# Performance work log

Hardware: AMD Instinct MI355X
Metric: run time of the kernel (lower is better)

Reference implementation:

```python
import math
import jax, jax.numpy as jnp
import numpy as np
from jax import lax

PATCHSIZE = [(8, 8), (4, 4), (2, 2), (1, 1)]  # (width, height)
BN_EPS = 1e-5


def setup_inputs() -> dict:
    key = jax.random.key(0)
    ks = jax.random.split(key, 6)
    b, c, h, w = 4, 256, 64, 64
    s = 1.0 / math.sqrt(c)
    return {
        "x": jax.random.normal(ks[0], (b, c, h, w), jnp.float32),
        "Wq": jax.random.normal(ks[1], (c, c), jnp.float32) * s,
        "bq": jnp.zeros((c,), jnp.float32),
        "Wk": jax.random.normal(ks[2], (c, c), jnp.float32) * s,
        "bk": jnp.zeros((c,), jnp.float32),
        "Wv": jax.random.normal(ks[3], (c, c), jnp.float32) * s,
        "bv": jnp.zeros((c,), jnp.float32),
        "Wo": jax.random.normal(ks[4], (c, c, 3, 3), jnp.float32) * (1.0 / math.sqrt(c * 9)),
        "bo": jnp.zeros((c,), jnp.float32),
        "gamma": jnp.ones((c,), jnp.float32),
        "beta": jnp.zeros((c,), jnp.float32),
        "running_mean": jnp.zeros((c,), jnp.float32),
        "running_var": jnp.ones((c,), jnp.float32),
    }


def _patch_attention(q, k, v, ph, pw):
    # q/k/v: [b, dk, h, w] -> tokens [b, n_patches, dk*ph*pw]
    b, dk, h, w = q.shape
    oh, ow = h // ph, w // pw

    def to_tok(t):
        t = t.reshape(b, dk, oh, ph, ow, pw)
        return t.transpose(0, 2, 4, 1, 3, 5).reshape(b, oh * ow, dk * ph * pw)

    qt, kt, vt = to_tok(q), to_tok(k), to_tok(v)
    scale = 1.0 / math.sqrt(dk * ph * pw)
    scores = jnp.einsum("bnd,bmd->bnm", qt, kt) * scale
    y = jnp.einsum("bnm,bmd->bnd", jax.nn.softmax(scores, axis=-1), vt)
    y = y.reshape(b, oh, ow, dk, ph, pw).transpose(0, 3, 1, 4, 2, 5)
    return y.reshape(b, dk, h, w)


def reference(x, Wq, bq, Wk, bk, Wv, bv, Wo, bo, gamma, beta, running_mean, running_var):
    b, c, h, w = x.shape
    nh = len(PATCHSIZE)
    dk = c // nh
    # 1x1 conv QKV projections
    q = jnp.einsum("bchw,oc->bohw", x, Wq) + bq[:, None, None]
    k = jnp.einsum("bchw,oc->bohw", x, Wk) + bk[:, None, None]
    v = jnp.einsum("bchw,oc->bohw", x, Wv) + bv[:, None, None]
    outs = []
    for i, (pw_, ph_) in enumerate(PATCHSIZE):
        sl = slice(i * dk, (i + 1) * dk)
        outs.append(_patch_attention(q[:, sl], k[:, sl], v[:, sl], ph_, pw_))
    out = jnp.concatenate(outs, axis=1)
    # 3x3 conv, SAME padding
    out = lax.conv_general_dilated(
        out, Wo, window_strides=(1, 1), padding="SAME",
        dimension_numbers=("NCHW", "OIHW", "NCHW"),
    ) + bo[:, None, None]
    # BatchNorm2d (inference-mode with running stats)
    inv = lax.rsqrt(running_var + BN_EPS)
    out = (out - running_mean[:, None, None]) * (gamma * inv)[:, None, None] + beta[:, None, None]
    # LeakyReLU(0.2)
    return jnp.where(out >= 0, out, 0.2 * out)
```

## Files before the change

kernel.cpp:

```cpp
#include <hip/hip_runtime.h>
#include <hip/hip_bf16.h>
#include <math.h>

#define NPOS 4096
#define CPB  1048576
#define QOFF  ((size_t)0)
#define KOFF  ((size_t)4194304)
#define VOFF  ((size_t)8388608)
#define AOFF  ((size_t)12582912)
#define S0OFF ((size_t)16777216)
#define WTOFF ((size_t)21250048)
#define QTOFF   S0OFF
#define KTOFF   (S0OFF + (size_t)2097152)
#define SP0OFF  (S0OFF + (size_t)4194304)
#define VTOFF   QOFF
#define ML3OFF  (QOFF + (size_t)2097152)
#define ML2OFF  (QOFF + (size_t)2228224)
#define OP3OFF  KOFF
#define SP1OFF  VOFF
#define OP2OFF  (VOFF + (size_t)2097152)

#define LOG2E 1.44269504088896340736f

typedef __attribute__((ext_vector_type(8))) short bf16x8;
typedef __attribute__((ext_vector_type(4))) float f32x4;

static __device__ __forceinline__ unsigned short f2bf(float f) {
  __hip_bfloat16 h = __float2bfloat16(f);
  unsigned short u;
  __builtin_memcpy(&u, &h, sizeof(u));
  return u;
}

static __device__ __forceinline__ float bf2f(unsigned short u) {
  unsigned v = ((unsigned)u) << 16;
  float f;
  __builtin_memcpy(&f, &v, sizeof(f));
  return f;
}

template<int PH, int PW>
__device__ __forceinline__ void scat_qk(unsigned short* __restrict__ dst,
                                        const unsigned short* __restrict__ Ac,
                                        int gh, int tid) {
  constexpr int PP = PH * PW, OW = 64 / PW, D = 64 * PP;
  int po = gh / PH, y = gh % PH;
  constexpr int NCH = 64 * OW;
#pragma unroll
  for (int j = 0; j < NCH / 256; ++j) {
    int id = j * 256 + tid;
    int c = id / OW, qo = id % OW;
    int tt = po * OW + qo;
    unsigned short buf[PW];
#pragma unroll
    for (int x = 0; x < PW; ++x) buf[x] = Ac[c * 66 + qo * PW + x];
    unsigned short* dp = &dst[(size_t)tt * D + c * PP + y * PW];
    if constexpr (PW == 8)      { uint4 v;  __builtin_memcpy(&v, buf, 16); *(uint4*)dp = v; }
    else if constexpr (PW == 4) { uint2 v;  __builtin_memcpy(&v, buf, 8);  *(uint2*)dp = v; }
    else                        { unsigned v; __builtin_memcpy(&v, buf, 4); *(unsigned*)dp = v; }
  }
}

template<int PH, int PW>
__device__ __forceinline__ void scat_v(unsigned short* __restrict__ dst,
                                       const unsigned short* __restrict__ Ac,
                                       int gh, int tid) {
  constexpr int PP = PH * PW, OW = 64 / PW, NT = 4096 / PP;
  int po = gh / PH, y = gh % PH;
  constexpr int NCH = 64 * PW;
  constexpr int CPT = (NCH + 255) / 256;
#pragma unroll
  for (int j = 0; j < CPT; ++j) {
    int id = j * 256 + tid;
    if (NCH < 256 && id >= NCH) break;
    int c = id / PW, x = id % PW;
    int d = c * PP + y * PW + x;
    unsigned short* dp = &dst[(size_t)d * NT + po * OW];
#pragma unroll
    for (int s = 0; s < OW; s += 8) {
      unsigned short buf[8];
#pragma unroll
      for (int e = 0; e < 8; ++e) buf[e] = Ac[c * 66 + (s + e) * PW + x];
      uint4 v; __builtin_memcpy(&v, buf, 16);
      *(uint4*)&dp[s] = v;
    }
  }
}

__global__ __launch_bounds__(256) void qkv_fused(
    const float* __restrict__ x,
    const float* __restrict__ Wq, const float* __restrict__ Wk, const float* __restrict__ Wv,
    const float* __restrict__ bq, const float* __restrict__ bk, const float* __restrict__ bv,
    const float* __restrict__ Wo, unsigned short* __restrict__ W2,
    unsigned short* __restrict__ qt, unsigned short* __restrict__ kt_,
    unsigned short* __restrict__ vt) {
  if (blockIdx.z == 12) {
    int o = blockIdx.y * 64 + blockIdx.x;
    size_t base = (size_t)o * 2304;
#pragma unroll
    for (int r = 0; r < 9; ++r) {
      int rr = r * 256 + threadIdx.x;
      int c = rr / 9, k = rr % 9;
      W2[(size_t)k * 65536 + (size_t)o * 256 + c] = f2bf(Wo[base + rr]);
    }
    return;
  }
  int b = blockIdx.z / 3, t = blockIdx.z % 3;
  const float* W    = (t == 0) ? Wq : (t == 1) ? Wk : Wv;
  const float* bias = (t == 0) ? bq : (t == 1) ? bk : bv;
  int h = blockIdx.y, gh = blockIdx.x;
  int o0 = h * 64, p0 = gh * 64;
  __shared__ unsigned short smem[2 * 64 * 72];
  unsigned short* Wt = smem;
  unsigned short* Xs = smem + 64 * 72;
  int tid = threadIdx.x;
  int wv = tid >> 6, l = tid & 63;
  int lg = l >> 4, ll = l & 15;
  f32x4 acc[4];
#pragma unroll
  for (int mi = 0; mi < 4; ++mi) acc[mi] = (f32x4){0.f, 0.f, 0.f, 0.f};

  int wol = tid >> 2, wcp = (tid & 3) * 16;
  int xcc = tid >> 6, xpz = tid & 63;

  for (int c0 = 0; c0 < 256; c0 += 64) {
    __syncthreads();
#pragma unroll
    for (int u = 0; u < 4; ++u) {
      float4 w4 = *(const float4*)&W[(size_t)(o0 + wol) * 256 + c0 + wcp + u * 4];
      ushort4 pk;
      pk.x = f2bf(w4.x); pk.y = f2bf(w4.y); pk.z = f2bf(w4.z); pk.w = f2bf(w4.w);
      *(ushort4*)&Wt[wol * 72 + wcp + u * 4] = pk;
    }
#pragma unroll
    for (int r = 0; r < 16; ++r) {
      int c = xcc * 16 + r;
      Xs[xpz * 72 + c] = f2bf(x[(size_t)b * CPB + (size_t)(c0 + c) * NPOS + p0 + xpz]);
    }
    __syncthreads();
#pragma unroll
    for (int ks = 0; ks < 2; ++ks) {
      bf16x8 xb = *(const bf16x8*)&Xs[(wv * 16 + ll) * 72 + ks * 32 + lg * 8];
#pragma unroll
      for (int mi = 0; mi < 4; ++mi) {
        bf16x8 wa = *(const bf16x8*)&Wt[(mi * 16 + ll) * 72 + ks * 32 + lg * 8];
        acc[mi] = __builtin_amdgcn_mfma_f32_16x16x32_bf16(wa, xb, acc[mi], 0, 0, 0);
      }
    }
  }
  __syncthreads();
  float qs = 1.0f;
  if (t == 0) qs = (h == 2) ? 0.0625f * LOG2E : (h == 3) ? 0.125f * LOG2E : 1.0f;
  unsigned short* Ac = smem;
#pragma unroll
  for (int mi = 0; mi < 4; ++mi)
#pragma unroll
    for (int r = 0; r < 4; ++r) {
      int ol = mi * 16 + lg * 4 + r;
      Ac[ol * 66 + wv * 16 + ll] = f2bf((acc[mi][r] + bias[o0 + ol]) * qs);
    }
  __syncthreads();
  if (t < 2) {
    unsigned short* dst = (t == 0 ? qt : kt_) + ((size_t)b * 4 + h) * 262144;
    switch (h) {
      case 0: scat_qk<8, 8>(dst, Ac, gh, tid); break;
      case 1: scat_qk<4, 4>(dst, Ac, gh, tid); break;
      case 2: scat_qk<2, 2>(dst, Ac, gh, tid); break;
      default: {
        int p = tid >> 2, c0 = (tid & 3) * 16;
        unsigned short buf[16];
#pragma unroll
        for (int e = 0; e < 16; ++e) buf[e] = Ac[(c0 + e) * 66 + p];
        uint4 v0, v1;
        __builtin_memcpy(&v0, buf, 16);
        __builtin_memcpy(&v1, buf + 8, 16);
        uint4* d4 = (uint4*)&dst[(size_t)(gh * 64 + p) * 64 + c0];
        d4[0] = v0; d4[1] = v1;
      } break;
    }
  } else {
    unsigned short* dst = vt + ((size_t)b * 4 + h) * 262144;
    switch (h) {
      case 0: scat_v<8, 8>(dst, Ac, gh, tid); break;
      case 1: scat_v<4, 4>(dst, Ac, gh, tid); break;
      case 2: scat_v<2, 2>(dst, Ac, gh, tid); break;
      default: {
        if (tid < 64) {
#pragma unroll
          for (int seg = 0; seg < 8; ++seg) {
            unsigned short buf[8];
#pragma unroll
            for (int e = 0; e < 8; ++e) buf[e] = Ac[tid * 66 + seg * 8 + e];
            uint4 v; __builtin_memcpy(&v, buf, 16);
            *(uint4*)&dst[(size_t)tid * 4096 + gh * 64 + seg * 8] = v;
          }
        }
      } break;
    }
  }
}

template<int NTOK, int DDIM, int NSPLIT, int KVB, int PH, int PW, int HEAD>
__device__ __forceinline__ void flash_body(
    unsigned char* smem, int b, int q0, int split,
    const unsigned short* __restrict__ qt, const unsigned short* __restrict__ kt_,
    const unsigned short* __restrict__ vt, unsigned short* __restrict__ opart,
    float* __restrict__ ml, unsigned short* __restrict__ attbf) {
  constexpr int KSTR = DDIM + 8;
  constexpr int VSTR = KVB + 8;
  constexpr int NT   = KVB / 16;
  constexpr int KCH  = DDIM / 32;
  constexpr int PKS  = KVB / 32;
  constexpr int OCG  = DDIM / 16;
  constexpr int PP = PH * PW, OW = 64 / PW;
  const unsigned short* Q = qt + ((size_t)b * 4 + HEAD) * 262144;
  const unsigned short* K = kt_ + ((size_t)b * 4 + HEAD) * 262144;
  const unsigned short* V = vt + ((size_t)b * 4 + HEAD) * 262144;
  unsigned short* Ks = (unsigned short*)smem;
  unsigned short* Vs = Ks + KVB * KSTR;
  unsigned short* Psw = Vs + DDIM * VSTR;
  int tid = threadIdx.x;
  int wv = tid >> 6, l = tid & 63;
  int lg = l >> 4, ll = l & 15;
  int qw = q0 + wv * 16;
  unsigned short* Ps = Psw + wv * 16 * VSTR;

  bf16x8 qf[KCH];
#pragma unroll
  for (int kc = 0; kc < KCH; ++kc)
    qf[kc] = *(const bf16x8*)&Q[(size_t)(qw + ll) * DDIM + kc * 32 + lg * 8];

  bf16x8 onesf;
#pragma unroll
  for (int e = 0; e < 8; ++e) onesf[e] = (short)0x3F80;

  f32x4 lacc = (f32x4){0.f, 0.f, 0.f, 0.f};
  f32x4 o_acc[OCG];
#pragma unroll
  for (int c = 0; c < OCG; ++c) o_acc[c] = (f32x4){0.f, 0.f, 0.f, 0.f};

  for (int kt0 = split * (NTOK / NSPLIT); kt0 < (split + 1) * (NTOK / NSPLIT); kt0 += KVB) {
    __syncthreads();
#pragma unroll
    for (int i = 0; i < KVB * DDIM / 2048; ++i) {
      int u = i * 256 + tid;
      int key = u / (DDIM / 8), part = u % (DDIM / 8);
      *(uint4*)&Ks[key * KSTR + part * 8] =
          *(const uint4*)&K[(size_t)(kt0 + key) * DDIM + part * 8];
    }
#pragma unroll
    for (int i = 0; i < KVB * DDIM / 2048; ++i) {
      int u = i * 256 + tid;
      int d = u / (KVB / 8), part = u % (KVB / 8);
      *(uint4*)&Vs[d * VSTR + part * 8] =
          *(const uint4*)&V[(size_t)d * NTOK + kt0 + part * 8];
    }
    __syncthreads();
    f32x4 s_acc[NT];
#pragma unroll
    for (int n = 0; n < NT; ++n) s_acc[n] = (f32x4){0.f, 0.f, 0.f, 0.f};
    __builtin_amdgcn_s_setprio(1);
#pragma unroll
    for (int n = 0; n < NT; ++n)
#pragma unroll
      for (int kc = 0; kc < KCH; ++kc) {
        bf16x8 kf = *(const bf16x8*)&Ks[(n * 16 + ll) * KSTR + kc * 32 + lg * 8];
        s_acc[n] = __builtin_amdgcn_mfma_f32_16x16x32_bf16(qf[kc], kf, s_acc[n], 0, 0, 0);
      }
    __builtin_amdgcn_s_setprio(0);
#pragma unroll
    for (int n = 0; n < NT; ++n)
#pragma unroll
      for (int r = 0; r < 4; ++r)
        Ps[(lg * 4 + r) * VSTR + n * 16 + ll] = f2bf(exp2f(s_acc[n][r]));
    __builtin_amdgcn_s_setprio(1);
#pragma unroll
    for (int pk = 0; pk < PKS; ++pk) {
      bf16x8 pa = *(const bf16x8*)&Ps[ll * VSTR + pk * 32 + lg * 8];
      lacc = __builtin_amdgcn_mfma_f32_16x16x32_bf16(pa, onesf, lacc, 0, 0, 0);
#pragma unroll
      for (int c = 0; c < OCG; ++c) {
        bf16x8 vf = *(const bf16x8*)&Vs[(c * 16 + ll) * VSTR + pk * 32 + lg * 8];
        o_acc[c] = __builtin_amdgcn_mfma_f32_16x16x32_bf16(pa, vf, o_acc[c], 0, 0, 0);
      }
    }
    __builtin_amdgcn_s_setprio(0);
  }
  if constexpr (NSPLIT > 1) {
    size_t ob = (size_t)(b * NSPLIT + split) * NTOK;
#pragma unroll
    for (int r = 0; r < 4; ++r) {
      int q = qw + lg * 4 + r;
#pragma unroll
      for (int c = 0; c < OCG; ++c)
        opart[(ob + q) * DDIM + c * 16 + ll] = f2bf(o_acc[c][r]);
      if (ll == 0) {
        ml[(ob + q) * 2]     = 0.f;
        ml[(ob + q) * 2 + 1] = lacc[r];
      }
    }
  } else {
#pragma unroll
    for (int r = 0; r < 4; ++r) {
      float inv = 1.0f / lacc[r];
      int q = qw + lg * 4 + r;
      int po = q / OW, qo = q % OW;
#pragma unroll
      for (int c = 0; c < OCG; ++c) {
        int d = c * 16 + ll;
        int ch = d / PP, rem = d % PP, y = rem / PW, x = rem % PW;
        int pos = (po * PH + y) * 64 + qo * PW + x;
        attbf[((size_t)b * NPOS + pos) * 256 + HEAD * 64 + ch] = f2bf(o_acc[c][r] * inv);
      }
    }
  }
}

__device__ __forceinline__ void flash3_dbuf(
    unsigned char* smem, int b, int q0, int split,
    const unsigned short* __restrict__ qt, const unsigned short* __restrict__ kt_,
    const unsigned short* __restrict__ vt, unsigned short* __restrict__ opart,
    float* __restrict__ ml) {
  const unsigned short* Q = qt + ((size_t)b * 4 + 3) * 262144;
  const unsigned short* K = kt_ + ((size_t)b * 4 + 3) * 262144;
  const unsigned short* V = vt + ((size_t)b * 4 + 3) * 262144;
  int tid = threadIdx.x;
  int wv = tid >> 6, l = tid & 63;
  int lg = l >> 4, ll = l & 15;
  int qw = q0 + wv * 16;
  unsigned short* Ps = (unsigned short*)(smem + 36864) + wv * 16 * 72;

  bf16x8 qf[2];
  qf[0] = *(const bf16x8*)&Q[(size_t)(qw + ll) * 64 + lg * 8];
  qf[1] = *(const bf16x8*)&Q[(size_t)(qw + ll) * 64 + 32 + lg * 8];

  bf16x8 onesf;
#pragma unroll
  for (int e = 0; e < 8; ++e) onesf[e] = (short)0x3F80;

  f32x4 lacc = (f32x4){0.f, 0.f, 0.f, 0.f};
  f32x4 o_acc[4];
#pragma unroll
  for (int c = 0; c < 4; ++c) o_acc[c] = (f32x4){0.f, 0.f, 0.f, 0.f};

  const int kstart = split * 1024, kend = kstart + 1024;

  {
    unsigned short* Kd = (unsigned short*)smem;
    unsigned short* Vd = Kd + 4608;
#pragma unroll
    for (int i = 0; i < 2; ++i) {
      int u = i * 256 + tid, row = u >> 3, part = u & 7;
      *(uint4*)&Kd[row * 72 + part * 8] =
          *(const uint4*)&K[(size_t)(kstart + row) * 64 + part * 8];
      *(uint4*)&Vd[row * 72 + part * 8] =
          *(const uint4*)&V[(size_t)row * 4096 + kstart + part * 8];
    }
  }
  __syncthreads();

  int cur = 0;
  for (int kt0 = kstart; kt0 < kend; kt0 += 64) {
    const bool more = (kt0 + 64) < kend;
    if (more) {
      unsigned short* Kd = (unsigned short*)(smem + (cur ^ 1) * 18432);
      unsigned short* Vd = Kd + 4608;
#pragma unroll
      for (int i = 0; i < 2; ++i) {
        int u = i * 256 + tid, row = u >> 3, part = u & 7;
        *(uint4*)&Kd[row * 72 + part * 8] =
            *(const uint4*)&K[(size_t)(kt0 + 64 + row) * 64 + part * 8];
        *(uint4*)&Vd[row * 72 + part * 8] =
            *(const uint4*)&V[(size_t)row * 4096 + (kt0 + 64) + part * 8];
      }
    }
    unsigned short* Kc = (unsigned short*)(smem + cur * 18432);
    unsigned short* Vc = Kc + 4608;
    f32x4 s_acc[4];
#pragma unroll
    for (int n = 0; n < 4; ++n) s_acc[n] = (f32x4){0.f, 0.f, 0.f, 0.f};
    __builtin_amdgcn_s_setprio(1);
#pragma unroll
    for (int n = 0; n < 4; ++n)
#pragma unroll
      for (int kc = 0; kc < 2; ++kc) {
        bf16x8 kf = *(const bf16x8*)&Kc[(n * 16 + ll) * 72 + kc * 32 + lg * 8];
        s_acc[n] = __builtin_amdgcn_mfma_f32_16x16x32_bf16(qf[kc], kf, s_acc[n], 0, 0, 0);
      }
    __builtin_amdgcn_s_setprio(0);
#pragma unroll
    for (int n = 0; n < 4; ++n)
#pragma unroll
      for (int r = 0; r < 4; ++r)
        Ps[(lg * 4 + r) * 72 + n * 16 + ll] = f2bf(exp2f(s_acc[n][r]));
    __builtin_amdgcn_s_setprio(1);
#pragma unroll
    for (int pk = 0; pk < 2; ++pk) {
      bf16x8 pa = *(const bf16x8*)&Ps[ll * 72 + pk * 32 + lg * 8];
      lacc = __builtin_amdgcn_mfma_f32_16x16x32_bf16(pa, onesf, lacc, 0, 0, 0);
#pragma unroll
      for (int c = 0; c < 4; ++c) {
        bf16x8 vf = *(const bf16x8*)&Vc[(c * 16 + ll) * 72 + pk * 32 + lg * 8];
        o_acc[c] = __builtin_amdgcn_mfma_f32_16x16x32_bf16(pa, vf, o_acc[c], 0, 0, 0);
      }
    }
    __builtin_amdgcn_s_setprio(0);
    __syncthreads();
    cur ^= 1;
  }
  size_t ob = (size_t)(b * 4 + split) * 4096;
#pragma unroll
  for (int r = 0; r < 4; ++r) {
    int q = qw + lg * 4 + r;
#pragma unroll
    for (int c = 0; c < 4; ++c)
      opart[(ob + q) * 64 + c * 16 + ll] = f2bf(o_acc[c][r]);
    if (ll == 0) {
      ml[(ob + q) * 2]     = 0.f;
      ml[(ob + q) * 2 + 1] = lacc[r];
    }
  }
}

__device__ __forceinline__ void h0_score_body(unsigned char* smem, int b, int ds,
                                              const unsigned short* __restrict__ qt,
                                              const unsigned short* __restrict__ kt_,
                                              float* __restrict__ spart) {
  const unsigned short* Q = qt + ((size_t)b * 4 + 0) * 262144;
  const unsigned short* K = kt_ + ((size_t)b * 4 + 0) * 262144;
  unsigned short* Qc = (unsigned short*)smem;
  unsigned short* Kc = Qc + 64 * 72;
  int tid = threadIdx.x;
  int wv = tid >> 6, l = tid & 63;
  int lg = l >> 4, ll = l & 15;
  f32x4 s_acc[4];
#pragma unroll
  for (int n = 0; n < 4; ++n) s_acc[n] = (f32x4){0.f, 0.f, 0.f, 0.f};
  for (int ch = 0; ch < 8; ++ch) {
    int d0 = ds * 512 + ch * 64;
    __syncthreads();
#pragma unroll
    for (int i = 0; i < 2; ++i) {
      int u = i * 256 + tid, row = u >> 3, part = u & 7;
      *(uint4*)&Qc[row * 72 + part * 8] = *(const uint4*)&Q[(size_t)row * 4096 + d0 + part * 8];
      *(uint4*)&Kc[row * 72 + part * 8] = *(const uint4*)&K[(size_t)row * 4096 + d0 + part * 8];
    }
    __syncthreads();
#pragma unroll
    for (int n = 0; n < 4; ++n)
#pragma unroll
      for (int ks = 0; ks < 2; ++ks) {
        bf16x8 qa = *(const bf16x8*)&Qc[(wv * 16 + ll) * 72 + ks * 32 + lg * 8];
        bf16x8 kf = *(const bf16x8*)&Kc[(n * 16 + ll) * 72 + ks * 32 + lg * 8];
        s_acc[n] = __builtin_amdgcn_mfma_f32_16x16x32_bf16(qa, kf, s_acc[n], 0, 0, 0);
      }
  }
#pragma unroll
  for (int n = 0; n < 4; ++n)
#pragma unroll
    for (int r = 0; r < 4; ++r)
      spart[(((size_t)b * 8 + ds) * 64 + (wv * 16 + lg * 4 + r)) * 64 + n * 16 + ll] =
          s_acc[n][r];
}

__device__ __forceinline__ void h1_score_body(unsigned char* smem, int b, int qtile, int ds,
                                              const unsigned short* __restrict__ qt,
                                              const unsigned short* __restrict__ kt_,
                                              float* __restrict__ spart) {
  int q0 = qtile * 64, dbase = ds * 128;
  const unsigned short* Q = qt + ((size_t)b * 4 + 1) * 262144;
  const unsigned short* K = kt_ + ((size_t)b * 4 + 1) * 262144;
  unsigned short* Qc = (unsigned short*)smem;
  unsigned short* Kc = Qc + 64 * 72;
  int tid = threadIdx.x;
  int wv = tid >> 6, l = tid & 63;
  int lg = l >> 4, ll = l & 15;
  f32x4 s_acc[16];
#pragma unroll
  for (int n = 0; n < 16; ++n) s_acc[n] = (f32x4){0.f, 0.f, 0.f, 0.f};
  for (int dc = 0; dc < 2; ++dc) {
    int d0 = dbase + dc * 64;
    __syncthreads();
#pragma unroll
    for (int i = 0; i < 2; ++i) {
      int u = i * 256 + tid, row = u >> 3, part = u & 7;
      *(uint4*)&Qc[row * 72 + part * 8] =
          *(const uint4*)&Q[(size_t)(q0 + row) * 1024 + d0 + part * 8];
    }
#pragma unroll
    for (int i = 0; i < 8; ++i) {
      int u = i * 256 + tid, row = u >> 3, part = u & 7;
      *(uint4*)&Kc[row * 72 + part * 8] =
          *(const uint4*)&K[(size_t)row * 1024 + d0 + part * 8];
    }
    __syncthreads();
#pragma unroll
    for (int ks = 0; ks < 2; ++ks) {
      bf16x8 qa = *(const bf16x8*)&Qc[(wv * 16 + ll) * 72 + ks * 32 + lg * 8];
#pragma unroll
      for (int n = 0; n < 16; ++n) {
        bf16x8 kf = *(const bf16x8*)&Kc[(n * 16 + ll) * 72 + ks * 32 + lg * 8];
        s_acc[n] = __builtin_amdgcn_mfma_f32_16x16x32_bf16(qa, kf, s_acc[n], 0, 0, 0);
      }
    }
  }
#pragma unroll
  for (int n = 0; n < 16; ++n)
#pragma unroll
    for (int r = 0; r < 4; ++r) {
      int q = q0 + wv * 16 + lg * 4 + r;
      spart[(((size_t)b * 8 + ds) * 256 + q) * 256 + n * 16 + ll] = s_acc[n][r];
    }
}

__global__ __launch_bounds__(256) void attn_all(
    const unsigned short* __restrict__ qt, const unsigned short* __restrict__ kt_,
    const unsigned short* __restrict__ vt,
    unsigned short* __restrict__ op2, float* __restrict__ ml2,
    unsigned short* __restrict__ op3, float* __restrict__ ml3,
    float* __restrict__ sp0, float* __restrict__ sp1,
    unsigned short* __restrict__ attbf) {
  __shared__ __align__(16) unsigned char smem[46080];
  int bid = blockIdx.x;
  if (bid < 1024) {
    int b = bid & 3, qy = (bid >> 2) & 63, split = bid >> 8;
    flash3_dbuf(smem, b, qy * 64, split, qt, kt_, vt, op3, ml3);
  } else if (bid < 1152) {
    int r = bid - 1024;
    int b = r & 3, qy = (r >> 2) & 15, split = r >> 6;
    flash_body<1024, 256, 2, 32, 2, 2, 2>(smem, b, qy * 64, split, qt, kt_, vt,
                                          op2, ml2, attbf);
  } else {
    int r = bid - 1152;
    if (r < 32) h0_score_body(smem, r >> 3, r & 7, qt, kt_, sp0);
    else {
      int rr = r - 32;
      h1_score_body(smem, rr >> 5, (rr >> 3) & 3, rr & 7, qt, kt_, sp1);
    }
  }
}

__device__ __forceinline__ void h0_pv_body(unsigned char* smem, int b, int ds,
                                           const float* __restrict__ spart,
                                           const unsigned short* __restrict__ vt,
                                           unsigned short* __restrict__ attbf) {
  const unsigned short* V = vt + ((size_t)b * 4 + 0) * 262144;
  float* S = (float*)smem;
  unsigned short* Ps = (unsigned short*)(smem + 16640);
  unsigned short* Vc = Ps + 64 * 72;
  int tid = threadIdx.x;
  int wv = tid >> 6, l = tid & 63;
  int lg = l >> 4, ll = l & 15;
#pragma unroll
  for (int i = 0; i < 16; ++i) {
    int idx = i * 256 + tid, q = idx >> 6, k = idx & 63;
    float s = 0.f;
#pragma unroll
    for (int sl = 0; sl < 8; ++sl)
      s += spart[(((size_t)b * 8 + sl) * 64 + q) * 64 + k];
    S[q * 65 + k] = s;
  }
  __syncthreads();
  for (int rr = 0; rr < 16; ++rr) {
    int row = wv * 16 + rr;
    float v = S[row * 65 + l] * 0.015625f;
    float m = v;
#pragma unroll
    for (int d = 32; d >= 1; d >>= 1) m = fmaxf(m, __shfl_xor(m, d));
    float p = __expf(v - m);
    float su = p;
#pragma unroll
    for (int d = 32; d >= 1; d >>= 1) su += __shfl_xor(su, d);
    Ps[row * 72 + l] = f2bf(p / su);
  }
  __syncthreads();
  for (int ch = 0; ch < 8; ++ch) {
    int d0 = ds * 512 + ch * 64;
    __syncthreads();
#pragma unroll
    for (int i = 0; i < 2; ++i) {
      int u = i * 256 + tid, row = u >> 3, part = u & 7;
      *(uint4*)&Vc[row * 72 + part * 8] =
          *(const uint4*)&V[(size_t)(d0 + row) * 64 + part * 8];
    }
    __syncthreads();
    f32x4 o[4];
#pragma unroll
    for (int cg = 0; cg < 4; ++cg) o[cg] = (f32x4){0.f, 0.f, 0.f, 0.f};
#pragma unroll
    for (int cg = 0; cg < 4; ++cg)
#pragma unroll
      for (int ks = 0; ks < 2; ++ks) {
        bf16x8 pa = *(const bf16x8*)&Ps[(wv * 16 + ll) * 72 + ks * 32 + lg * 8];
        bf16x8 vf = *(const bf16x8*)&Vc[(cg * 16 + ll) * 72 + ks * 32 + lg * 8];
        o[cg] = __builtin_amdgcn_mfma_f32_16x16x32_bf16(pa, vf, o[cg], 0, 0, 0);
      }
#pragma unroll
    for (int cg = 0; cg < 4; ++cg)
#pragma unroll
      for (int r = 0; r < 4; ++r) {
        int q = wv * 16 + lg * 4 + r;
        int d = d0 + cg * 16 + ll;
        int c = d >> 6, rem = d & 63, y = rem >> 3, x = rem & 7;
        int po = q >> 3, qo = q & 7;
        int pos = (po * 8 + y) * 64 + qo * 8 + x;
        attbf[((size_t)b * NPOS + pos) * 256 + c] = f2bf(o[cg][r]);
      }
  }
}

__device__ __forceinline__ void h1_pv_body(unsigned char* smem, int b, int qtile, int vs,
                                           const float* __restrict__ spart,
                                           const unsigned short* __restrict__ vt,
                                           unsigned short* __restrict__ attbf) {
  int q0 = qtile * 64, dv0 = vs * 128;
  const unsigned short* V = vt + ((size_t)b * 4 + 1) * 262144;
  unsigned short* Ps = (unsigned short*)smem;
  unsigned short* Vs = Ps + 64 * 264;
  int tid = threadIdx.x;
  int wv = tid >> 6, l = tid & 63;
  int lg = l >> 4, ll = l & 15;
  for (int rr = 0; rr < 16; ++rr) {
    int row = q0 + wv * 16 + rr;
    float sv[4];
#pragma unroll
    for (int c4 = 0; c4 < 4; ++c4) {
      float s = 0.f;
#pragma unroll
      for (int sl = 0; sl < 8; ++sl)
        s += spart[(((size_t)b * 8 + sl) * 256 + row) * 256 + c4 * 64 + l];
      sv[c4] = s * 0.03125f;
    }
    float m = fmaxf(fmaxf(sv[0], sv[1]), fmaxf(sv[2], sv[3]));
#pragma unroll
    for (int d = 32; d >= 1; d >>= 1) m = fmaxf(m, __shfl_xor(m, d));
    float p[4], su = 0.f;
#pragma unroll
    for (int c4 = 0; c4 < 4; ++c4) { p[c4] = __expf(sv[c4] - m); su += p[c4]; }
#pragma unroll
    for (int d = 32; d >= 1; d >>= 1) su += __shfl_xor(su, d);
    float inv = 1.0f / su;
#pragma unroll
    for (int c4 = 0; c4 < 4; ++c4)
      Ps[(wv * 16 + rr) * 264 + c4 * 64 + l] = f2bf(p[c4] * inv);
  }
  for (int vc = 0; vc < 4; ++vc) {
    int d0 = dv0 + vc * 32;
    __syncthreads();
#pragma unroll
    for (int i = 0; i < 4; ++i) {
      int u = i * 256 + tid, row = u >> 5, part = u & 31;
      *(uint4*)&Vs[row * 264 + part * 8] =
          *(const uint4*)&V[(size_t)(d0 + row) * 256 + part * 8];
    }
    __syncthreads();
    f32x4 o[2];
    o[0] = (f32x4){0.f, 0.f, 0.f, 0.f};
    o[1] = (f32x4){0.f, 0.f, 0.f, 0.f};
#pragma unroll
    for (int ks = 0; ks < 8; ++ks) {
      bf16x8 pa = *(const bf16x8*)&Ps[(wv * 16 + ll) * 264 + ks * 32 + lg * 8];
#pragma unroll
      for (int cg = 0; cg < 2; ++cg) {
        bf16x8 vf = *(const bf16x8*)&Vs[(cg * 16 + ll) * 264 + ks * 32 + lg * 8];
        o[cg] = __builtin_amdgcn_mfma_f32_16x16x32_bf16(pa, vf, o[cg], 0, 0, 0);
      }
    }
#pragma unroll
    for (int cg = 0; cg < 2; ++cg)
#pragma unroll
      for (int r = 0; r < 4; ++r) {
        int q = q0 + wv * 16 + lg * 4 + r;
        int d = d0 + cg * 16 + ll;
        int c = d >> 4, rem = d & 15, y = rem >> 2, x = rem & 3;
        int po = q >> 4, qo = q & 15;
        int pos = (po * 4 + y) * 64 + qo * 4 + x;
        attbf[((size_t)b * NPOS + pos) * 256 + 64 + c] = f2bf(o[cg][r]);
      }
  }
}

__global__ __launch_bounds__(256) void finish_all(
    const float* __restrict__ sp0, const float* __restrict__ sp1,
    const unsigned short* __restrict__ op2, const float* __restrict__ ml2,
    const unsigned short* __restrict__ op3, const float* __restrict__ ml3,
    const unsigned short* __restrict__ vt, unsigned short* __restrict__ attbf) {
  __shared__ __align__(16) unsigned char smem[50688];
  int bid = blockIdx.x;
  if (bid < 32) { h0_pv_body(smem, bid >> 3, bid & 7, sp0, vt, attbf); return; }
  if (bid < 160) {
    int r = bid - 32;
    h1_pv_body(smem, r >> 5, (r >> 3) & 3, r & 7, sp1, vt, attbf);
    return;
  }
  int cb = bid - 160;
  if (cb < 4096) {
    int b = cb >> 10, q = cb & 1023;
    int d = threadIdx.x;
    float num = 0.f, den = 0.f;
#pragma unroll
    for (int s = 0; s < 2; ++s) {
      den += ml2[((size_t)(b * 2 + s) * 1024 + q) * 2 + 1];
      num += bf2f(op2[((size_t)(b * 2 + s) * 1024 + q) * 256 + d]);
    }
    int c = d >> 2, rem = d & 3, y = rem >> 1, x = rem & 1;
    int po = q >> 5, qo = q & 31;
    int pos = (po * 2 + y) * 64 + qo * 2 + x;
    attbf[((size_t)b * NPOS + pos) * 256 + 128 + c] = f2bf(num / den);
  } else {
    cb -= 4096;
    int b = cb >> 10, qt4 = cb & 1023;
    int q = qt4 * 4 + (threadIdx.x >> 6), ch = threadIdx.x & 63;
    float num = 0.f, den = 0.f;
#pragma unroll
    for (int s = 0; s < 4; ++s) {
      den += ml3[((size_t)(b * 4 + s) * 4096 + q) * 2 + 1];
      num += bf2f(op3[((size_t)(b * 4 + s) * 4096 + q) * 64 + ch]);
    }
    attbf[((size_t)b * 4096 + q) * 256 + 192 + ch] = f2bf(num / den);
  }
}

__global__ __launch_bounds__(512) void conv_mfma(
    const unsigned short* __restrict__ attbf, const unsigned short* __restrict__ w2,
    const float* __restrict__ bo, const float* __restrict__ gamma,
    const float* __restrict__ beta, const float* __restrict__ rmean,
    const float* __restrict__ rvar, float* __restrict__ out) {
  int hq = blockIdx.x, ot = blockIdx.y, b = blockIdx.z;
  int h0 = hq * 4, o0 = ot * 64;
  __shared__ unsigned short As[4 * 66 * 72];
  __shared__ unsigned short Ws[3 * 64 * 72];
  int tid = threadIdx.x;
  int wi = tid >> 6, l = tid & 63;
  int hrow = wi >> 1, wseg = wi & 1;
  int lg = l >> 4, ll = l & 15;
  const size_t attb = (size_t)b * NPOS * 256;
  f32x4 acc[4][2];
#pragma unroll
  for (int mi = 0; mi < 4; ++mi)
#pragma unroll
    for (int ni = 0; ni < 2; ++ni) acc[mi][ni] = (f32x4){0.f, 0.f, 0.f, 0.f};

  for (int dy = 0; dy < 3; ++dy) {
    for (int c0 = 0; c0 < 256; c0 += 64) {
      __syncthreads();
      if (tid < 256) {
        int rowl = tid >> 6, w = tid & 63;
        int ghh = h0 + dy - 1 + rowl;
        uint4 z = make_uint4(0u, 0u, 0u, 0u);
        uint4 a[8];
        if (ghh >= 0 && ghh < 64) {
          const uint4* src = (const uint4*)(attbf + attb + ((size_t)(ghh * 64 + w) * 256 + c0));
#pragma unroll
          for (int q = 0; q < 8; ++q) a[q] = src[q];
        } else {
#pragma unroll
          for (int q = 0; q < 8; ++q) a[q] = z;
        }
        uint4* dst = (uint4*)&As[(rowl * 66 + 1 + w) * 72];
#pragma unroll
        for (int q = 0; q < 8; ++q) dst[q] = a[q];
        if (w == 0 || w == 63) {
          uint4* dz = (uint4*)&As[(rowl * 66 + ((w == 0) ? 0 : 65)) * 72];
#pragma unroll
          for (int q = 0; q < 8; ++q) dz[q] = z;
        }
      } else {
        int p = tid - 256;
        int dx = p >> 6, ol = p & 63;
        if (dx < 3) {
          const uint4* src = (const uint4*)(w2 + ((size_t)(dy * 3 + dx) * 65536 +
                                                  (size_t)(o0 + ol) * 256 + c0));
          uint4* dst = (uint4*)&Ws[(dx * 64 + ol) * 72];
#pragma unroll
          for (int q = 0; q < 8; ++q) dst[q] = src[q];
        }
      }
      __syncthreads();
#pragma unroll
      for (int dx = 0; dx < 3; ++dx) {
#pragma unroll
        for (int ks = 0; ks < 2; ++ks) {
          bf16x8 af[4];
#pragma unroll
          for (int mi = 0; mi < 4; ++mi)
            af[mi] = *(const bf16x8*)&Ws[(dx * 64 + mi * 16 + ll) * 72 + ks * 32 + lg * 8];
#pragma unroll
          for (int ni = 0; ni < 2; ++ni) {
            bf16x8 bfr = *(const bf16x8*)&As[(hrow * 66 + wseg * 32 + ni * 16 + ll + dx) * 72 +
                                             ks * 32 + lg * 8];
#pragma unroll
            for (int mi = 0; mi < 4; ++mi)
              acc[mi][ni] = __builtin_amdgcn_mfma_f32_16x16x32_bf16(af[mi], bfr, acc[mi][ni],
                                                                    0, 0, 0);
          }
        }
      }
    }
  }
  int h = h0 + hrow;
#pragma unroll
  for (int mi = 0; mi < 4; ++mi) {
#pragma unroll
    for (int r = 0; r < 4; ++r) {
      int o = o0 + mi * 16 + lg * 4 + r;
      float g  = gamma[o] * rsqrtf(rvar[o] + 1e-5f);
      float bb = (bo[o] - rmean[o]) * g + beta[o];
#pragma unroll
      for (int ni = 0; ni < 2; ++ni) {
        float zv = acc[mi][ni][r] * g + bb;
        zv = (zv >= 0.f) ? zv : 0.2f * zv;
        out[((size_t)(b * 256 + o)) * NPOS + h * 64 + wseg * 32 + ni * 16 + ll] = zv;
      }
    }
  }
}

extern "C" void kernel_launch(void* const* d_in, const int* in_sizes, int n_in,
                              void* d_out, int out_size, void* d_ws, size_t ws_size,
                              hipStream_t stream) {
  (void)in_sizes; (void)n_in; (void)out_size; (void)ws_size;
  const float* x     = (const float*)d_in[0];
  const float* Wq    = (const float*)d_in[1];
  const float* bq    = (const float*)d_in[2];
  const float* Wk    = (const float*)d_in[3];
  const float* bk    = (const float*)d_in[4];
  const float* Wv    = (const float*)d_in[5];
  const float* bv    = (const float*)d_in[6];
  const float* Wo    = (const float*)d_in[7];
  const float* bo    = (const float*)d_in[8];
  const float* gamma = (const float*)d_in[9];
  const float* beta  = (const float*)d_in[10];
  const float* rmean = (const float*)d_in[11];
  const float* rvar  = (const float*)d_in[12];
  float* ws  = (float*)d_ws;
  float* out = (float*)d_out;
  unsigned short* attbf = (unsigned short*)(ws + AOFF);
  unsigned short* w2bf  = (unsigned short*)(ws + WTOFF);
  unsigned short* qt    = (unsigned short*)(ws + QTOFF);
  unsigned short* kt    = (unsigned short*)(ws + KTOFF);
  unsigned short* vt    = (unsigned short*)(ws + VTOFF);
  unsigned short* op2   = (unsigned short*)(ws + OP2OFF);
  unsigned short* op3   = (unsigned short*)(ws + OP3OFF);

  qkv_fused<<<dim3(64, 4, 13), 256, 0, stream>>>(x, Wq, Wk, Wv, bq, bk, bv,
                                                 Wo, w2bf, qt, kt, vt);

  attn_all<<<1312, 256, 0, stream>>>(qt, kt, vt,
                                     op2, ws + ML2OFF,
                                     op3, ws + ML3OFF,
                                     ws + SP0OFF, ws + SP1OFF, attbf);

  finish_all<<<8352, 256, 0, stream>>>(ws + SP0OFF, ws + SP1OFF,
                                       op2, ws + ML2OFF,
                                       op3, ws + ML3OFF, vt, attbf);

  conv_mfma<<<dim3(16, 4, 4), 512, 0, stream>>>(attbf, w2bf, bo, gamma, beta,
                                                rmean, rvar, out);
}
```

Before: 183.4 us.

## Process two 64-query tiles per block in head-3 flash attention to reuse K/V tiles

Each head-3 flash attention block now handles 128 queries as two 64-query sub-tiles sharing the same staged K/V shared-memory tiles. This halves the number of head-3 blocks and the global-to-LDS K/V traffic per query, and the grid shrinks from 1312 to 800 blocks. In exchange each thread holds twice the accumulators, which raises register pressure and may lower occupancy, and fewer blocks means less parallelism to hide latency.

After: 176.7 us. 3.6% less time.

```diff
diff --git a/kernel.cpp b/kernel.cpp
--- a/kernel.cpp
+++ b/kernel.cpp
@@ -327,21 +327,28 @@
   int tid = threadIdx.x;
   int wv = tid >> 6, l = tid & 63;
   int lg = l >> 4, ll = l & 15;
-  int qw = q0 + wv * 16;
+  int qwA = q0 + wv * 16;
+  int qwB = qwA + 64;
   unsigned short* Ps = (unsigned short*)(smem + 36864) + wv * 16 * 72;
 
-  bf16x8 qf[2];
-  qf[0] = *(const bf16x8*)&Q[(size_t)(qw + ll) * 64 + lg * 8];
-  qf[1] = *(const bf16x8*)&Q[(size_t)(qw + ll) * 64 + 32 + lg * 8];
+  bf16x8 qfA[2], qfB[2];
+  qfA[0] = *(const bf16x8*)&Q[(size_t)(qwA + ll) * 64 + lg * 8];
+  qfA[1] = *(const bf16x8*)&Q[(size_t)(qwA + ll) * 64 + 32 + lg * 8];
+  qfB[0] = *(const bf16x8*)&Q[(size_t)(qwB + ll) * 64 + lg * 8];
+  qfB[1] = *(const bf16x8*)&Q[(size_t)(qwB + ll) * 64 + 32 + lg * 8];
 
   bf16x8 onesf;
 #pragma unroll
   for (int e = 0; e < 8; ++e) onesf[e] = (short)0x3F80;
 
-  f32x4 lacc = (f32x4){0.f, 0.f, 0.f, 0.f};
-  f32x4 o_acc[4];
-#pragma unroll
-  for (int c = 0; c < 4; ++c) o_acc[c] = (f32x4){0.f, 0.f, 0.f, 0.f};
+  f32x4 laccA = (f32x4){0.f, 0.f, 0.f, 0.f};
+  f32x4 laccB = (f32x4){0.f, 0.f, 0.f, 0.f};
+  f32x4 o_accA[4], o_accB[4];
+#pragma unroll
+  for (int c = 0; c < 4; ++c) {
+    o_accA[c] = (f32x4){0.f, 0.f, 0.f, 0.f};
+    o_accB[c] = (f32x4){0.f, 0.f, 0.f, 0.f};
+  }
 
   const int kstart = split * 1024, kend = kstart + 1024;
 
@@ -376,48 +383,87 @@
     }
     unsigned short* Kc = (unsigned short*)(smem + cur * 18432);
     unsigned short* Vc = Kc + 4608;
-    f32x4 s_acc[4];
-#pragma unroll
-    for (int n = 0; n < 4; ++n) s_acc[n] = (f32x4){0.f, 0.f, 0.f, 0.f};
-    __builtin_amdgcn_s_setprio(1);
-#pragma unroll
-    for (int n = 0; n < 4; ++n)
-#pragma unroll
-      for (int kc = 0; kc < 2; ++kc) {
-        bf16x8 kf = *(const bf16x8*)&Kc[(n * 16 + ll) * 72 + kc * 32 + lg * 8];
-        s_acc[n] = __builtin_amdgcn_mfma_f32_16x16x32_bf16(qf[kc], kf, s_acc[n], 0, 0, 0);
-      }
-    __builtin_amdgcn_s_setprio(0);
-#pragma unroll
-    for (int n = 0; n < 4; ++n)
-#pragma unroll
-      for (int r = 0; r < 4; ++r)
-        Ps[(lg * 4 + r) * 72 + n * 16 + ll] = f2bf(exp2f(s_acc[n][r]));
-    __builtin_amdgcn_s_setprio(1);
-#pragma unroll
-    for (int pk = 0; pk < 2; ++pk) {
-      bf16x8 pa = *(const bf16x8*)&Ps[ll * 72 + pk * 32 + lg * 8];
-      lacc = __builtin_amdgcn_mfma_f32_16x16x32_bf16(pa, onesf, lacc, 0, 0, 0);
-#pragma unroll
-      for (int c = 0; c < 4; ++c) {
-        bf16x8 vf = *(const bf16x8*)&Vc[(c * 16 + ll) * 72 + pk * 32 + lg * 8];
-        o_acc[c] = __builtin_amdgcn_mfma_f32_16x16x32_bf16(pa, vf, o_acc[c], 0, 0, 0);
-      }
-    }
-    __builtin_amdgcn_s_setprio(0);
+
+    {
+      f32x4 s_acc[4];
+#pragma unroll
+      for (int n = 0; n < 4; ++n) s_acc[n] = (f32x4){0.f, 0.f, 0.f, 0.f};
+      __builtin_amdgcn_s_setprio(1);
+#pragma unroll
+      for (int n = 0; n < 4; ++n)
+#pragma unroll
+        for (int kc = 0; kc < 2; ++kc) {
+          bf16x8 kf = *(const bf16x8*)&Kc[(n * 16 + ll) * 72 + kc * 32 + lg * 8];
+          s_acc[n] = __builtin_amdgcn_mfma_f32_16x16x32_bf16(qfA[kc], kf, s_acc[n], 0, 0, 0);
+        }
+      __builtin_amdgcn_s_setprio(0);
+#pragma unroll
+      for (int n = 0; n < 4; ++n)
+#pragma unroll
+        for (int r = 0; r < 4; ++r)
+          Ps[(lg * 4 + r) * 72 + n * 16 + ll] = f2bf(exp2f(s_acc[n][r]));
+      __builtin_amdgcn_s_setprio(1);
+#pragma unroll
+      for (int pk = 0; pk < 2; ++pk) {
+        bf16x8 pa = *(const bf16x8*)&Ps[ll * 72 + pk * 32 + lg * 8];
+        laccA = __builtin_amdgcn_mfma_f32_16x16x32_bf16(pa, onesf, laccA, 0, 0, 0);
+#pragma unroll
+        for (int c = 0; c < 4; ++c) {
+          bf16x8 vf = *(const bf16x8*)&Vc[(c * 16 + ll) * 72 + pk * 32 + lg * 8];
+          o_accA[c] = __builtin_amdgcn_mfma_f32_16x16x32_bf16(pa, vf, o_accA[c], 0, 0, 0);
+        }
+      }
+      __builtin_amdgcn_s_setprio(0);
+    }
+    {
+      f32x4 s_acc[4];
+#pragma unroll
+      for (int n = 0; n < 4; ++n) s_acc[n] = (f32x4){0.f, 0.f, 0.f, 0.f};
+      __builtin_amdgcn_s_setprio(1);
+#pragma unroll
+      for (int n = 0; n < 4; ++n)
+#pragma unroll
+        for (int kc = 0; kc < 2; ++kc) {
+          bf16x8 kf = *(const bf16x8*)&Kc[(n * 16 + ll) * 72 + kc * 32 + lg * 8];
+          s_acc[n] = __builtin_amdgcn_mfma_f32_16x16x32_bf16(qfB[kc], kf, s_acc[n], 0, 0, 0);
+        }
+      __builtin_amdgcn_s_setprio(0);
+#pragma unroll
+      for (int n = 0; n < 4; ++n)
+#pragma unroll
+        for (int r = 0; r < 4; ++r)
+          Ps[(lg * 4 + r) * 72 + n * 16 + ll] = f2bf(exp2f(s_acc[n][r]));
+      __builtin_amdgcn_s_setprio(1);
+#pragma unroll
+      for (int pk = 0; pk < 2; ++pk) {
+        bf16x8 pa = *(const bf16x8*)&Ps[ll * 72 + pk * 32 + lg * 8];
+        laccB = __builtin_amdgcn_mfma_f32_16x16x32_bf16(pa, onesf, laccB, 0, 0, 0);
+#pragma unroll
+        for (int c = 0; c < 4; ++c) {
+          bf16x8 vf = *(const bf16x8*)&Vc[(c * 16 + ll) * 72 + pk * 32 + lg * 8];
+          o_accB[c] = __builtin_amdgcn_mfma_f32_16x16x32_bf16(pa, vf, o_accB[c], 0, 0, 0);
+        }
+      }
+      __builtin_amdgcn_s_setprio(0);
+    }
     __syncthreads();
     cur ^= 1;
   }
   size_t ob = (size_t)(b * 4 + split) * 4096;
 #pragma unroll
   for (int r = 0; r < 4; ++r) {
-    int q = qw + lg * 4 + r;
-#pragma unroll
-    for (int c = 0; c < 4; ++c)
-      opart[(ob + q) * 64 + c * 16 + ll] = f2bf(o_acc[c][r]);
+    int qA = qwA + lg * 4 + r;
+    int qB = qwB + lg * 4 + r;
+#pragma unroll
+    for (int c = 0; c < 4; ++c) {
+      opart[(ob + qA) * 64 + c * 16 + ll] = f2bf(o_accA[c][r]);
+      opart[(ob + qB) * 64 + c * 16 + ll] = f2bf(o_accB[c][r]);
+    }
     if (ll == 0) {
-      ml[(ob + q) * 2]     = 0.f;
-      ml[(ob + q) * 2 + 1] = lacc[r];
+      ml[(ob + qA) * 2]     = 0.f;
+      ml[(ob + qA) * 2 + 1] = laccA[r];
+      ml[(ob + qB) * 2]     = 0.f;
+      ml[(ob + qB) * 2 + 1] = laccB[r];
     }
   }
 }
@@ -522,16 +568,16 @@
     unsigned short* __restrict__ attbf) {
   __shared__ __align__(16) unsigned char smem[46080];
   int bid = blockIdx.x;
-  if (bid < 1024) {
-    int b = bid & 3, qy = (bid >> 2) & 63, split = bid >> 8;
-    flash3_dbuf(smem, b, qy * 64, split, qt, kt_, vt, op3, ml3);
-  } else if (bid < 1152) {
-    int r = bid - 1024;
+  if (bid < 512) {
+    int b = bid & 3, qy = (bid >> 2) & 31, split = bid >> 7;
+    flash3_dbuf(smem, b, qy * 128, split, qt, kt_, vt, op3, ml3);
+  } else if (bid < 640) {
+    int r = bid - 512;
     int b = r & 3, qy = (r >> 2) & 15, split = r >> 6;
     flash_body<1024, 256, 2, 32, 2, 2, 2>(smem, b, qy * 64, split, qt, kt_, vt,
                                           op2, ml2, attbf);
   } else {
-    int r = bid - 1152;
+    int r = bid - 640;
     if (r < 32) h0_score_body(smem, r >> 3, r & 7, qt, kt_, sp0);
     else {
       int rr = r - 32;
@@ -846,10 +892,10 @@
   qkv_fused<<<dim3(64, 4, 13), 256, 0, stream>>>(x, Wq, Wk, Wv, bq, bk, bv,
                                                  Wo, w2bf, qt, kt, vt);
 
-  attn_all<<<1312, 256, 0, stream>>>(qt, kt, vt,
-                                     op2, ws + ML2OFF,
-                                     op3, ws + ML3OFF,
-                                     ws + SP0OFF, ws + SP1OFF, attbf);
+  attn_all<<<800, 256, 0, stream>>>(qt, kt, vt,
+                                    op2, ws + ML2OFF,
+                                    op3, ws + ML3OFF,
+                                    ws + SP0OFF, ws + SP1OFF, attbf);
 
   finish_all<<<8352, 256, 0, stream>>>(ws + SP0OFF, ws + SP1OFF,
                                        op2, ws + ML2OFF,
```
